# Optimization experiments

Hardware: AMD Instinct MI355X
Metric: run time of the kernel (lower is better)

## Reference

```python
import jax, jax.numpy as jnp
import numpy as np

B, N, D = 8, 1024, 768
H, Y, M = 12, 64, 3072  # heads, head_dim, hopfield memories (4*D)
STEPS = 12
ALPHA = 0.1
EPS = 1e-5


def setup_inputs() -> dict:
    key = jax.random.key(0)
    k0, k1, k2, k3 = jax.random.split(key, 4)
    return {
        "x": jax.random.normal(k0, (B, N, D), dtype=jnp.float32),
        "gamma": jnp.ones((D,), dtype=jnp.float32),
        "beta_ln": jnp.zeros((D,), dtype=jnp.float32),
        "Wq": jax.random.normal(k1, (H, Y, D), dtype=jnp.float32) / np.float32(np.sqrt(D)),
        "Wk": jax.random.normal(k2, (H, Y, D), dtype=jnp.float32) / np.float32(np.sqrt(D)),
        "xi": jax.random.normal(k3, (M, D), dtype=jnp.float32) / np.float32(np.sqrt(D)),
    }


def _layernorm(x, gamma, beta_ln):
    mu = jnp.mean(x, axis=-1, keepdims=True)
    var = jnp.var(x, axis=-1, keepdims=True)
    return gamma * (x - mu) * jax.lax.rsqrt(var + EPS) + beta_ln


def _energy(g, Wq, Wk, xi):
    # Energy attention: E^ATT = -(1/beta) * sum_{h,q} logsumexp_k(beta * <K_hk, Q_hq>)
    q = jnp.einsum('hyd,bnd->bhny', Wq, g)
    k = jnp.einsum('hyd,bnd->bhny', Wk, g)
    beta = jnp.asarray(1.0 / np.sqrt(Y), g.dtype)
    scores = beta * jnp.einsum('bhky,bhqy->bhkq', k, q)  # [B,H,N_k,N_q]
    e_att = -(1.0 / beta) * jnp.sum(jax.nn.logsumexp(scores, axis=2))
    # Hopfield energy: E^HN = -0.5 * sum relu(g @ xi^T)^2
    h = jnp.einsum('bnd,md->bnm', g, xi)
    e_hn = -0.5 * jnp.sum(jnp.square(jax.nn.relu(h)))
    return e_att + e_hn


def reference(x, gamma, beta_ln, Wq, Wk, xi):
    grad_e = jax.grad(_energy)
    def step(xc, _):
        g = _layernorm(xc, gamma, beta_ln)
        # gradient taken at g (not chained through LayerNorm), then SGD update
        xc = xc - ALPHA * grad_e(g, Wq, Wk, xi)
        return xc, None
    out, _ = jax.lax.scan(step, x, None, length=STEPS)
    return out
```

## Files before the change

### kernel.cpp

```cpp
#include <hip/hip_runtime.h>
#include <math.h>

#define H_ 12
#define STEPS_ 12
#define ALPHA_ 0.1f
#define EPS_ 1e-5f
#define BETA_ 0.125f
#define B2L_ 0.1803368801111204f
#define L2E_ 1.4426950408889634f
#define NTOK 8192

typedef unsigned short u16;
typedef __attribute__((ext_vector_type(8))) u16 u16x8;
typedef __attribute__((ext_vector_type(4))) u16 u16x4;
typedef __attribute__((ext_vector_type(4))) float f32x4;
typedef __attribute__((ext_vector_type(8))) __bf16 bf16x8;

#define MFMA __builtin_amdgcn_mfma_f32_16x16x32_bf16
#define EXP2F(x) __builtin_amdgcn_exp2f(x)

__device__ __forceinline__ u16 f2bf(float x) {
    unsigned u = __float_as_uint(x);
    u += 0x7FFFu + ((u >> 16) & 1u);
    return (u16)(u >> 16);
}
__device__ __forceinline__ float bf2f(u16 u) {
    return __uint_as_float(((unsigned)u) << 16);
}
__device__ __forceinline__ u16 f2bf_rz(float x) {
    return (u16)(__float_as_uint(x) >> 16);
}

__device__ __forceinline__ void gl2lds16(const u16* gsrc, u16* ldst) {
    __builtin_amdgcn_global_load_lds(
        (const __attribute__((address_space(1))) void*)gsrc,
        (__attribute__((address_space(3))) void*)ldst, 16, 0, 0);
}

#define RAW_BARRIER()   asm volatile("s_barrier" ::: "memory")
#define WAIT_VM(n)      asm volatile("s_waitcnt vmcnt(" #n ")" ::: "memory")
#define SCHED_FENCE()   __builtin_amdgcn_sched_barrier(0)

__global__ __launch_bounds__(256) void ln_kernel(const float* __restrict__ x,
    const float* __restrict__ gamma, const float* __restrict__ beta,
    u16* __restrict__ g)
{
    int row = blockIdx.x;
    const float* xr = x + (size_t)row * 768;
    u16* gr = g + (size_t)row * 768;
    int t = threadIdx.x;
    float v0 = xr[t], v1 = xr[t + 256], v2 = xr[t + 512];
    float s = v0 + v1 + v2;
    #pragma unroll
    for (int off = 32; off > 0; off >>= 1) s += __shfl_down(s, off);
    __shared__ float red[8];
    int wid = t >> 6, lane = t & 63;
    if (lane == 0) red[wid] = s;
    __syncthreads();
    if (t == 0) red[0] = (red[0] + red[1] + red[2] + red[3]) * (1.0f / 768.0f);
    __syncthreads();
    float mu = red[0];
    float d0 = v0 - mu, d1 = v1 - mu, d2 = v2 - mu;
    float ss = d0*d0 + d1*d1 + d2*d2;
    #pragma unroll
    for (int off = 32; off > 0; off >>= 1) ss += __shfl_down(ss, off);
    if (lane == 0) red[4 + wid] = ss;
    __syncthreads();
    if (t == 0) red[4] = rsqrtf((red[4] + red[5] + red[6] + red[7]) * (1.0f / 768.0f) + EPS_);
    __syncthreads();
    float rs = red[4];
    gr[t]       = f2bf(gamma[t]       * d0 * rs + beta[t]);
    gr[t + 256] = f2bf(gamma[t + 256] * d1 * rs + beta[t + 256]);
    gr[t + 512] = f2bf(gamma[t + 512] * d2 * rs + beta[t + 512]);
}

__global__ __launch_bounds__(192) void reduce_ln(const u16* __restrict__ part,
    float* __restrict__ xc, const float* __restrict__ gamma,
    const float* __restrict__ beta, u16* __restrict__ g)
{
    int row = blockIdx.x, t = threadIdx.x;
    const u16x4* p0 = (const u16x4*)(part + (size_t)row * 768);
    const u16x4* p1 = (const u16x4*)(part + (size_t)(8192 + row) * 768);
    f32x4* xr = (f32x4*)(xc + (size_t)row * 768);
    f32x4 v = xr[t];
    u16x4 a = p0[t], b = p1[t];
    #pragma unroll
    for (int e = 0; e < 4; ++e) v[e] = fmaf(ALPHA_, bf2f(a[e]) + bf2f(b[e]), v[e]);
    xr[t] = v;
    float s = (v[0] + v[1]) + (v[2] + v[3]);
    #pragma unroll
    for (int off = 32; off > 0; off >>= 1) s += __shfl_down(s, off);
    __shared__ float red[8];
    int wid = t >> 6, lane = t & 63;
    if (lane == 0) red[wid] = s;
    __syncthreads();
    if (t == 0) red[0] = (red[0] + red[1] + red[2]) * (1.0f / 768.0f);
    __syncthreads();
    float mu = red[0];
    f32x4 d;
    #pragma unroll
    for (int e = 0; e < 4; ++e) d[e] = v[e] - mu;
    float ss = (d[0]*d[0] + d[1]*d[1]) + (d[2]*d[2] + d[3]*d[3]);
    #pragma unroll
    for (int off = 32; off > 0; off >>= 1) ss += __shfl_down(ss, off);
    if (lane == 0) red[4 + wid] = ss;
    __syncthreads();
    if (t == 0) red[4] = rsqrtf((red[4] + red[5] + red[6]) * (1.0f / 768.0f) + EPS_);
    __syncthreads();
    float rs = red[4];
    const f32x4 gm = *(const f32x4*)&gamma[t * 4];
    const f32x4 bt = *(const f32x4*)&beta[t * 4];
    u16x4 o;
    #pragma unroll
    for (int e = 0; e < 4; ++e) o[e] = f2bf(fmaf(gm[e], d[e] * rs, bt[e]));
    *(u16x4*)&g[(size_t)row * 768 + t * 4] = o;
}

__global__ __launch_bounds__(256) void convert_bf(const float* __restrict__ src,
                                                  u16* __restrict__ dst, int n4)
{
    int i = blockIdx.x * 256 + threadIdx.x;
    if (i < n4) {
        f32x4 v = *(const f32x4*)&src[i * 4];
        u16x4 o;
        #pragma unroll
        for (int e = 0; e < 4; ++e) o[e] = f2bf(v[e]);
        *(u16x4*)&dst[i * 4] = o;
    }
}

__global__ __launch_bounds__(256) void transpose_bf(const float* __restrict__ Wq,
    const float* __restrict__ Wk, const float* __restrict__ xi, u16* __restrict__ out)
{
    __shared__ float tile[64][65];
    int rb = blockIdx.x * 64, cb = blockIdx.y * 64;
    const float* src;
    if (rb < 768) src = Wq + (size_t)rb * 768;
    else if (rb < 1536) src = Wk + (size_t)(rb - 768) * 768;
    else src = xi + (size_t)(rb - 1536) * 768;
    int t = threadIdx.x;
    #pragma unroll
    for (int it = 0; it < 4; ++it) {
        int r = (t >> 4) + 16 * it;
        f32x4 v = *(const f32x4*)&src[(size_t)r * 768 + cb + (t & 15) * 4];
        #pragma unroll
        for (int e = 0; e < 4; ++e) tile[r][(t & 15) * 4 + e] = v[e];
    }
    __syncthreads();
    #pragma unroll
    for (int it = 0; it < 4; ++it) {
        int cl = (t >> 4) + 16 * it;
        u16x4 o;
        #pragma unroll
        for (int e = 0; e < 4; ++e) o[e] = f2bf(tile[(t & 15) * 4 + e][cl]);
        *(u16x4*)&out[(size_t)(cb + cl) * 4608 + rb + (t & 15) * 4] = o;
    }
}


__global__ __launch_bounds__(512) void gemm_fwd(
    const u16* __restrict__ A,
    const u16* __restrict__ Bt,
    u16* __restrict__ qkb, u16* __restrict__ qkT, u16* __restrict__ midb)
{
    __shared__ __align__(16) u16 S[2][28672];
    const int t = threadIdx.x, w = t >> 6, l = t & 63, g = l >> 4, cid = l & 15;
    const int lr = l & 15, lc = l >> 4;
    const int wm = w >> 2, wn = w & 3;
    const int flat = blockIdx.x;
    const int xcd = flat & 7, slot = flat >> 3;
    const int nid = slot >> 2, mloc = slot & 3;
    const int bm = (xcd * 4 + mloc) * 256;
    const int bn = nid * 192;
    const int NT = 12;

    const u16* aS[4]; int ldA[4];
    #pragma unroll
    for (int j = 0; j < 4; ++j) {
        int rf = 2 * w + (j >> 1), kh = j & 1;
        aS[j] = A + (size_t)(bm + 16 * rf + lr) * 768 + 32 * kh + 8 * lc;
        ldA[j] = rf * 1024 + kh * 512 + l * 8;
    }
    const u16* bS[3]; int ldB[3];
    #pragma unroll
    for (int j = 0; j < 3; ++j) {
        int c = 3 * w + j, rf = c >> 1, kh = c & 1;
        bS[j] = Bt + (size_t)(bn + 16 * rf + lr) * 768 + 32 * kh + 8 * lc;
        ldB[j] = 16384 + rf * 1024 + kh * 512 + l * 8;
    }

    f32x4 acc[8][3] = {};
    bf16x8 afr[4][2], b0[2][2], b1[2];

    #pragma unroll
    for (int j = 0; j < 3; ++j) gl2lds16(bS[j], &S[0][ldB[j]]);
    #pragma unroll
    for (int j = 0; j < 4; ++j) gl2lds16(aS[j], &S[0][ldA[j]]);
    #pragma unroll
    for (int j = 0; j < 3; ++j) gl2lds16(bS[j] + 64, &S[1][ldB[j]]);
    WAIT_VM(3); RAW_BARRIER();

    #pragma unroll 1
    for (int tt = 0; tt < NT; ++tt) {
        const int bf = tt & 1, ob = bf ^ 1;
        const u16* Sa = &S[bf][0];
        const u16* Sb = &S[bf][16384];
        #define LDS_A(ii, hh) (*(const bf16x8*)&Sa[((wm * 8 + (ii)) * 128 + (hh) * 64 + l) * 8])
        #define LDS_B(jj, hh) (*(const bf16x8*)&Sb[((3 * wn + (jj)) * 128 + (hh) * 64 + l) * 8])
        #define MM(ii, jj, BF0, BF1) { \
            acc[ii][jj] = MFMA(afr[(ii) & 3][0], BF0, acc[ii][jj], 0, 0, 0); \
            acc[ii][jj] = MFMA(afr[(ii) & 3][1], BF1, acc[ii][jj], 0, 0, 0); }
        #pragma unroll
        for (int i = 0; i < 4; ++i) { afr[i][0] = LDS_A(i, 0); afr[i][1] = LDS_A(i, 1); }
        #pragma unroll
        for (int j = 0; j < 2; ++j) { b0[j][0] = LDS_B(j, 0); b0[j][1] = LDS_B(j, 1); }
        b1[0] = LDS_B(2, 0); b1[1] = LDS_B(2, 1);
        if (tt + 1 < NT) { gl2lds16(aS[0] + 64 * (tt + 1), &S[ob][ldA[0]]);
                           gl2lds16(aS[1] + 64 * (tt + 1), &S[ob][ldA[1]]);
                           gl2lds16(aS[2] + 64 * (tt + 1), &S[ob][ldA[2]]);
                           gl2lds16(aS[3] + 64 * (tt + 1), &S[ob][ldA[3]]); }
        RAW_BARRIER();
        __builtin_amdgcn_s_setprio(1);
        #pragma unroll
        for (int i = 0; i < 4; ++i) {
            MM(i, 0, b0[0][0], b0[0][1]);
            MM(i, 1, b0[1][0], b0[1][1]);
            MM(i, 2, b1[0],    b1[1]);
        }
        __builtin_amdgcn_s_setprio(0);
        SCHED_FENCE(); RAW_BARRIER();
        #pragma unroll
        for (int i = 0; i < 4; ++i) { afr[i][0] = LDS_A(4 + i, 0); afr[i][1] = LDS_A(4 + i, 1); }
        if (tt + 2 < NT) { gl2lds16(bS[0] + 64 * (tt + 2), &S[bf][ldB[0]]);
                           gl2lds16(bS[1] + 64 * (tt + 2), &S[bf][ldB[1]]);
                           gl2lds16(bS[2] + 64 * (tt + 2), &S[bf][ldB[2]]); }
        RAW_BARRIER();
        __builtin_amdgcn_s_setprio(1);
        #pragma unroll
        for (int i = 0; i < 4; ++i) {
            MM(4 + i, 0, b0[0][0], b0[0][1]);
            MM(4 + i, 1, b0[1][0], b0[1][1]);
            MM(4 + i, 2, b1[0],    b1[1]);
        }
        __builtin_amdgcn_s_setprio(0);
        SCHED_FENCE();
        if (tt < NT - 2)       { WAIT_VM(3); }
        else if (tt == NT - 2) { WAIT_VM(0); }
        RAW_BARRIER();
        #undef LDS_A
        #undef LDS_B
        #undef MM
    }

    if (bn < 1536) {
        int bidx = bm >> 10;
        #pragma unroll
        for (int i = 0; i < 8; ++i) {
            int tok = bm + wm * 128 + 16 * i + 4 * g;
            #pragma unroll
            for (int j = 0; j < 3; ++j) {
                int col = bn + wn * 48 + 16 * j + cid;
                int sel = col >= 768 ? 1 : 0;
                int cc = col - 768 * sel;
                int hh = cc >> 6, yy = cc & 63;
                u16x4 tv;
                #pragma unroll
                for (int r = 0; r < 4; ++r) {
                    u16 bv = f2bf(acc[i][j][r]);
                    tv[r] = bv;
                    qkb[(size_t)(tok + r) * 1536 + col] = bv;
                }
                *(u16x4*)&qkT[((((size_t)bidx * 12 + hh) * 2 + sel) * 64 + yy) * 1024 + (tok & 1023)] = tv;
            }
        }
    } else {
        #pragma unroll
        for (int i = 0; i < 8; ++i)
            #pragma unroll
            for (int r = 0; r < 4; ++r) {
                size_t row = bm + wm * 128 + 16 * i + 4 * g + r;
                #pragma unroll
                for (int j = 0; j < 3; ++j) {
                    int col = bn + wn * 48 + 16 * j + cid;
                    midb[row * 4608 + col] = f2bf(fmaxf(acc[i][j][r], 0.0f));
                }
            }
    }
}

__global__ __launch_bounds__(512) void gemm_upd(
    const u16* __restrict__ A,
    const u16* __restrict__ Bt,
    u16* __restrict__ part)
{
    __shared__ __align__(16) u16 S[2][28672];
    const int t = threadIdx.x, w = t >> 6, l = t & 63, g = l >> 4, cid = l & 15;
    const int lr = l & 15, lc = l >> 4;
    const int wm = w >> 2, wn = w & 3;
    const int flat = blockIdx.x;
    const int xcd = flat & 7, slot = flat >> 3;
    const int z = slot >> 4, rem = slot & 15;
    const int nid = rem >> 2, mloc = rem & 3;
    const int bm = (xcd * 4 + mloc) * 256, bn = nid * 192;
    const int kbeg = z * 2304;
    const int NT = 36;
    u16* out = part + (size_t)z * 8192 * 768;

    const u16* aS[4]; int ldA[4];
    #pragma unroll
    for (int j = 0; j < 4; ++j) {
        int rf = 2 * w + (j >> 1), kh = j & 1;
        aS[j] = A + (size_t)(bm + 16 * rf + lr) * 4608 + kbeg + 32 * kh + 8 * lc;
        ldA[j] = rf * 1024 + kh * 512 + l * 8;
    }
    const u16* bS[3]; int ldB[3];
    #pragma unroll
    for (int j = 0; j < 3; ++j) {
        int c = 3 * w + j, rf = c >> 1, kh = c & 1;
        bS[j] = Bt + (size_t)(bn + 16 * rf + lr) * 4608 + kbeg + 32 * kh + 8 * lc;
        ldB[j] = 16384 + rf * 1024 + kh * 512 + l * 8;
    }

    f32x4 acc[8][3] = {};
    bf16x8 afr[4][2], b0[2][2], b1[2];

    #pragma unroll
    for (int j = 0; j < 3; ++j) gl2lds16(bS[j], &S[0][ldB[j]]);
    #pragma unroll
    for (int j = 0; j < 4; ++j) gl2lds16(aS[j], &S[0][ldA[j]]);
    #pragma unroll
    for (int j = 0; j < 3; ++j) gl2lds16(bS[j] + 64, &S[1][ldB[j]]);
    WAIT_VM(3); RAW_BARRIER();

    #pragma unroll 1
    for (int tt = 0; tt < NT; ++tt) {
        const int bf = tt & 1, ob = bf ^ 1;
        const u16* Sa = &S[bf][0];
        const u16* Sb = &S[bf][16384];
        #define LDS_A(ii, hh) (*(const bf16x8*)&Sa[((wm * 8 + (ii)) * 128 + (hh) * 64 + l) * 8])
        #define LDS_B(jj, hh) (*(const bf16x8*)&Sb[((3 * wn + (jj)) * 128 + (hh) * 64 + l) * 8])
        #define MM(ii, jj, BF0, BF1) { \
            acc[ii][jj] = MFMA(afr[(ii) & 3][0], BF0, acc[ii][jj], 0, 0, 0); \
            acc[ii][jj] = MFMA(afr[(ii) & 3][1], BF1, acc[ii][jj], 0, 0, 0); }
        #pragma unroll
        for (int i = 0; i < 4; ++i) { afr[i][0] = LDS_A(i, 0); afr[i][1] = LDS_A(i, 1); }
        #pragma unroll
        for (int j = 0; j < 2; ++j) { b0[j][0] = LDS_B(j, 0); b0[j][1] = LDS_B(j, 1); }
        b1[0] = LDS_B(2, 0); b1[1] = LDS_B(2, 1);
        if (tt + 1 < NT) { gl2lds16(aS[0] + 64 * (tt + 1), &S[ob][ldA[0]]);
                           gl2lds16(aS[1] + 64 * (tt + 1), &S[ob][ldA[1]]);
                           gl2lds16(aS[2] + 64 * (tt + 1), &S[ob][ldA[2]]);
                           gl2lds16(aS[3] + 64 * (tt + 1), &S[ob][ldA[3]]); }
        RAW_BARRIER();
        __builtin_amdgcn_s_setprio(1);
        #pragma unroll
        for (int i = 0; i < 4; ++i) {
            MM(i, 0, b0[0][0], b0[0][1]);
            MM(i, 1, b0[1][0], b0[1][1]);
            MM(i, 2, b1[0],    b1[1]);
        }
        __builtin_amdgcn_s_setprio(0);
        SCHED_FENCE(); RAW_BARRIER();
        #pragma unroll
        for (int i = 0; i < 4; ++i) { afr[i][0] = LDS_A(4 + i, 0); afr[i][1] = LDS_A(4 + i, 1); }
        if (tt + 2 < NT) { gl2lds16(bS[0] + 64 * (tt + 2), &S[bf][ldB[0]]);
                           gl2lds16(bS[1] + 64 * (tt + 2), &S[bf][ldB[1]]);
                           gl2lds16(bS[2] + 64 * (tt + 2), &S[bf][ldB[2]]); }
        RAW_BARRIER();
        __builtin_amdgcn_s_setprio(1);
        #pragma unroll
        for (int i = 0; i < 4; ++i) {
            MM(4 + i, 0, b0[0][0], b0[0][1]);
            MM(4 + i, 1, b0[1][0], b0[1][1]);
            MM(4 + i, 2, b1[0],    b1[1]);
        }
        __builtin_amdgcn_s_setprio(0);
        SCHED_FENCE();
        if (tt < NT - 2)       { WAIT_VM(3); }
        else if (tt == NT - 2) { WAIT_VM(0); }
        RAW_BARRIER();
        #undef LDS_A
        #undef LDS_B
        #undef MM
    }

    #pragma unroll
    for (int i = 0; i < 8; ++i)
        #pragma unroll
        for (int r = 0; r < 4; ++r) {
            size_t row = bm + wm * 128 + 16 * i + 4 * g + r;
            #pragma unroll
            for (int j = 0; j < 3; ++j)
                out[row * 768 + bn + wn * 48 + 16 * j + cid] = f2bf(acc[i][j][r]);
        }
}

__global__ __launch_bounds__(256) void dq_kernel(const u16* __restrict__ qk,
    const u16* __restrict__ qkT, float* __restrict__ L, u16* __restrict__ mid)
{
    const int flat = blockIdx.x;
    const int xcd = flat & 7, slot = flat >> 3;
    const int bh = xcd * 12 + slot / 8;
    const int q0 = (slot % 8) << 7;
    const int b = bh / H_, h = bh % H_;
    const u16* qbase = qk + (size_t)b * 1024 * 1536 + h * 64;
    const u16* kbase = qbase + 768;
    const u16* ktg = qkT + ((size_t)bh * 2 + 1) * 64 * 1024;
    __shared__ __align__(16) u16 KB[2][8192];
    __shared__ __align__(16) u16 Ps[8192];
    const int t = threadIdx.x, w = t >> 6, l = t & 63, g = l >> 4, cid = l & 15;
    const int lr = l & 15, lc = l >> 4;

    #pragma unroll
    for (int h2 = 0; h2 < 2; ++h2)
        #pragma unroll
        for (int ch = 0; ch < 2; ++ch)
            gl2lds16(&qbase[(size_t)(q0 + 32 * w + 16 * h2 + lr) * 1536 + 32 * ch + 8 * lc],
                     &KB[0][(128 * (2 * w + h2) + 64 * ch + l) * 8]);
    __syncthreads();
    bf16x8 QF[2][2];
    #pragma unroll
    for (int jj = 0; jj < 2; ++jj)
        #pragma unroll
        for (int hh = 0; hh < 2; ++hh)
            QF[jj][hh] = *(const bf16x8*)&KB[0][(128 * (2 * w + jj) + 64 * hh + l) * 8];
    __syncthreads();

    auto stageK = [&](int buf, int kt) {
        #pragma unroll
        for (int ch = 0; ch < 2; ++ch) {
            gl2lds16(&kbase[(size_t)(kt * 64 + 16 * w + lr) * 1536 + 32 * ch + 8 * lc],
                     &KB[buf][(128 * w + 64 * ch + l) * 8]);
            gl2lds16(&ktg[(size_t)(16 * w + lr) * 1024 + kt * 64 + 32 * ch + 8 * lc],
                     &KB[buf][4096 + (128 * w + 64 * ch + l) * 8]);
        }
    };

    f32x4 acc[2][4] = {};
    float lrun[2] = {0.0f, 0.0f};

    stageK(0, 0); stageK(1, 1);
    #pragma unroll 1
    for (int kt = 0; kt < 16; ++kt) {
        if (kt == 15) { WAIT_VM(0); } else { WAIT_VM(4); }
        RAW_BARRIER();
        const int buf = kt & 1;
        const u16* Kn = &KB[buf][0];
        const u16* Kt = &KB[buf][4096];
        f32x4 s[4][2];
        #pragma unroll
        for (int i = 0; i < 4; ++i) {
            bf16x8 a0 = *(const bf16x8*)&Kn[(128 * i + l) * 8];
            bf16x8 a1 = *(const bf16x8*)&Kn[(128 * i + 64 + l) * 8];
            #pragma unroll
            for (int jj = 0; jj < 2; ++jj) {
                f32x4 z = {0.f, 0.f, 0.f, 0.f};
                z = MFMA(a0, QF[jj][0], z, 0, 0, 0);
                z = MFMA(a1, QF[jj][1], z, 0, 0, 0);
                s[i][jj] = z;
            }
        }
        #pragma unroll
        for (int jj = 0; jj < 2; ++jj) {
            float psum = 0.0f;
            #pragma unroll
            for (int i = 0; i < 4; ++i) {
                u16x4 pv;
                #pragma unroll
                for (int r = 0; r < 4; ++r) {
                    float p = EXP2F(s[i][jj][r] * B2L_);
                    psum += p;
                    pv[r] = f2bf_rz(p);
                }
                *(u16x4*)&Ps[(128 * (2 * w + jj) + 32 * i + 16 * (g >> 1) + cid) * 8 + 4 * (g & 1)] = pv;
            }
            psum += __shfl_xor(psum, 16);
            psum += __shfl_xor(psum, 32);
            lrun[jj] += psum;
        }
        #pragma unroll
        for (int jj = 0; jj < 2; ++jj) {
            bf16x8 p0 = *(const bf16x8*)&Ps[(128 * (2 * w + jj) + l) * 8];
            bf16x8 p1 = *(const bf16x8*)&Ps[(128 * (2 * w + jj) + 64 + l) * 8];
            #pragma unroll
            for (int j = 0; j < 4; ++j) {
                acc[jj][j] = MFMA(p0, *(const bf16x8*)&Kt[(128 * j + l) * 8], acc[jj][j], 0, 0, 0);
                acc[jj][j] = MFMA(p1, *(const bf16x8*)&Kt[(128 * j + 64 + l) * 8], acc[jj][j], 0, 0, 0);
            }
        }
        RAW_BARRIER();
        if (kt + 2 < 16) stageK(buf, kt + 2);
    }
    #pragma unroll
    for (int jj = 0; jj < 2; ++jj) {
        if (g == 0)
            L[(size_t)bh * 1024 + q0 + 32 * w + 16 * jj + cid] = __logf(lrun[jj]);
        float linv = 1.0f / lrun[jj];
        #pragma unroll
        for (int r = 0; r < 4; ++r) {
            float fr = __shfl(linv, 4 * g + r);
            int row = q0 + 32 * w + 16 * jj + 4 * g + r;
            #pragma unroll
            for (int j = 0; j < 4; ++j)
                mid[(size_t)(b * 1024 + row) * 4608 + h * 64 + 16 * j + cid] = f2bf(acc[jj][j][r] * fr);
        }
    }
}

__global__ __launch_bounds__(256) void dk_kernel(const u16* __restrict__ qk,
    const u16* __restrict__ qkT, const float* __restrict__ L, u16* __restrict__ mid)
{
    const int flat = blockIdx.x;
    const int xcd = flat & 7, slot = flat >> 3;
    const int bh = xcd * 12 + slot / 8;
    const int k0 = (slot % 8) << 7;
    const int b = bh / H_, h = bh % H_;
    const u16* qbase = qk + (size_t)b * 1024 * 1536 + h * 64;
    const u16* kbase = qbase + 768;
    const u16* qtg = qkT + ((size_t)bh * 2 + 0) * 64 * 1024;
    __shared__ __align__(16) u16 KB[2][8192];
    __shared__ __align__(16) u16 Ps[8192];
    const int t = threadIdx.x, w = t >> 6, l = t & 63, g = l >> 4, cid = l & 15;
    const int lr = l & 15, lc = l >> 4;

    #pragma unroll
    for (int h2 = 0; h2 < 2; ++h2)
        #pragma unroll
        for (int ch = 0; ch < 2; ++ch)
            gl2lds16(&kbase[(size_t)(k0 + 32 * w + 16 * h2 + lr) * 1536 + 32 * ch + 8 * lc],
                     &KB[0][(128 * (2 * w + h2) + 64 * ch + l) * 8]);
    __syncthreads();
    bf16x8 KF[2][2];
    #pragma unroll
    for (int jj = 0; jj < 2; ++jj)
        #pragma unroll
        for (int hh = 0; hh < 2; ++hh)
            KF[jj][hh] = *(const bf16x8*)&KB[0][(128 * (2 * w + jj) + 64 * hh + l) * 8];
    __syncthreads();

    auto stageQ = [&](int buf, int qt) {
        #pragma unroll
        for (int ch = 0; ch < 2; ++ch) {
            gl2lds16(&qbase[(size_t)(qt * 64 + 16 * w + lr) * 1536 + 32 * ch + 8 * lc],
                     &KB[buf][(128 * w + 64 * ch + l) * 8]);
            gl2lds16(&qtg[(size_t)(16 * w + lr) * 1024 + qt * 64 + 32 * ch + 8 * lc],
                     &KB[buf][4096 + (128 * w + 64 * ch + l) * 8]);
        }
    };

    f32x4 acc[2][4] = {};
    stageQ(0, 0); stageQ(1, 1);
    #pragma unroll 1
    for (int qt = 0; qt < 16; ++qt) {
        if (qt == 15) { WAIT_VM(0); } else { WAIT_VM(4); }
        RAW_BARRIER();
        const int buf = qt & 1;
        const u16* Qn = &KB[buf][0];
        const u16* Qt = &KB[buf][4096];
        #pragma unroll
        for (int i = 0; i < 4; ++i) {
            bf16x8 a0 = *(const bf16x8*)&Qn[(128 * i + l) * 8];
            bf16x8 a1 = *(const bf16x8*)&Qn[(128 * i + 64 + l) * 8];
            f32x4 lv = *(const f32x4*)&L[(size_t)bh * 1024 + qt * 64 + 16 * i + 4 * g];
            f32x4 lv2;
            #pragma unroll
            for (int r = 0; r < 4; ++r) lv2[r] = lv[r] * L2E_;
            #pragma unroll
            for (int jj = 0; jj < 2; ++jj) {
                f32x4 z = {0.f, 0.f, 0.f, 0.f};
                z = MFMA(a0, KF[jj][0], z, 0, 0, 0);
                z = MFMA(a1, KF[jj][1], z, 0, 0, 0);
                u16x4 pv;
                #pragma unroll
                for (int r = 0; r < 4; ++r)
                    pv[r] = f2bf_rz(EXP2F(fmaf(z[r], B2L_, -lv2[r])));
                *(u16x4*)&Ps[(128 * (2 * w + jj) + 32 * i + 16 * (g >> 1) + cid) * 8 + 4 * (g & 1)] = pv;
            }
        }
        #pragma unroll
        for (int jj = 0; jj < 2; ++jj) {
            bf16x8 p0 = *(const bf16x8*)&Ps[(128 * (2 * w + jj) + l) * 8];
            bf16x8 p1 = *(const bf16x8*)&Ps[(128 * (2 * w + jj) + 64 + l) * 8];
            #pragma unroll
            for (int j = 0; j < 4; ++j) {
                acc[jj][j] = MFMA(p0, *(const bf16x8*)&Qt[(128 * j + l) * 8], acc[jj][j], 0, 0, 0);
                acc[jj][j] = MFMA(p1, *(const bf16x8*)&Qt[(128 * j + 64 + l) * 8], acc[jj][j], 0, 0, 0);
            }
        }
        RAW_BARRIER();
        if (qt + 2 < 16) stageQ(buf, qt + 2);
    }
    #pragma unroll
    for (int jj = 0; jj < 2; ++jj)
        #pragma unroll
        for (int r = 0; r < 4; ++r) {
            int row = k0 + 32 * w + 16 * jj + 4 * g + r;
            #pragma unroll
            for (int j = 0; j < 4; ++j)
                mid[(size_t)(b * 1024 + row) * 4608 + 768 + h * 64 + 16 * j + cid] = f2bf(acc[jj][j][r]);
        }
}

extern "C" void kernel_launch(void* const* d_in, const int* in_sizes, int n_in,
                              void* d_out, int out_size, void* d_ws, size_t ws_size,
                              hipStream_t stream)
{
    const float* x     = (const float*)d_in[0];
    const float* gamma = (const float*)d_in[1];
    const float* betap = (const float*)d_in[2];
    const float* Wq    = (const float*)d_in[3];
    const float* Wk    = (const float*)d_in[4];
    const float* xi    = (const float*)d_in[5];
    float* xc = (float*)d_out;

    char* p = (char*)d_ws;
    u16* wcat_bf  = (u16*)p; p += (size_t)4608 * 768 * 2;
    u16* wcatT_bf = (u16*)p; p += (size_t)768 * 4608 * 2;
    u16* g_bf     = (u16*)p; p += (size_t)NTOK * 768 * 2;
    u16* qk_bf    = (u16*)p; p += (size_t)NTOK * 1536 * 2;
    u16* qkT_bf   = (u16*)p; p += (size_t)96 * 2 * 64 * 1024 * 2;
    u16* mid_bf   = (u16*)p; p += (size_t)NTOK * 4608 * 2;
    float* L      = (float*)p; p += (size_t)96 * 1024 * 4;
    u16* part = qk_bf;
    (void)ws_size; (void)in_sizes; (void)n_in; (void)out_size;

    hipMemcpyAsync(xc, x, (size_t)NTOK * 768 * 4, hipMemcpyDeviceToDevice, stream);

    convert_bf<<<576, 256, 0, stream>>>(Wq, wcat_bf, 147456);
    convert_bf<<<576, 256, 0, stream>>>(Wk, wcat_bf + 768 * 768, 147456);
    convert_bf<<<2304, 256, 0, stream>>>(xi, wcat_bf + 2 * 768 * 768, 589824);
    transpose_bf<<<dim3(72, 12), 256, 0, stream>>>(Wq, Wk, xi, wcatT_bf);

    ln_kernel<<<NTOK, 256, 0, stream>>>(x, gamma, betap, g_bf);

    for (int step = 0; step < STEPS_; ++step) {
        gemm_fwd<<<768, 512, 0, stream>>>(
            g_bf, wcat_bf, qk_bf, qkT_bf, mid_bf);
        dq_kernel<<<768, 256, 0, stream>>>(qk_bf, qkT_bf, L, mid_bf);
        dk_kernel<<<768, 256, 0, stream>>>(qk_bf, qkT_bf, L, mid_bf);
        gemm_upd<<<256, 512, 0, stream>>>(mid_bf, wcatT_bf, part);
        reduce_ln<<<NTOK, 192, 0, stream>>>(part, xc, gamma, betap, g_bf);
    }
}
```

Before: 3.036 ms.

## Make forward GEMM blocks loop over three N tiles in one launch

The forward GEMM now launches 256 blocks instead of 768. Each block walks three consecutive 192-column N tiles (576 columns) through one continuous software pipeline of 36 K-steps. Prefetch carries across tile boundaries, and the epilogue writes out and resets the accumulators after every 12 K-steps. The aim is to cut block launch and pipeline fill/drain overhead and to keep the A tile hot in cache, at the cost of fewer blocks (about one per CU) and epilogue stores that stall the pipeline mid-loop.

```diff
diff --git a/kernel.cpp b/kernel.cpp
--- a/kernel.cpp
+++ b/kernel.cpp
@@ -169,10 +169,11 @@
     const int wm = w >> 2, wn = w & 3;
     const int flat = blockIdx.x;
     const int xcd = flat & 7, slot = flat >> 3;
-    const int nid = slot >> 2, mloc = slot & 3;
+    const int ngrp = slot >> 2, mloc = slot & 3;
     const int bm = (xcd * 4 + mloc) * 256;
-    const int bn = nid * 192;
-    const int NT = 12;
+    const int bn0 = ngrp * 576;
+    const int NT = 36;
+    const int bidx = bm >> 10;
 
     const u16* aS[4]; int ldA[4];
     #pragma unroll
@@ -185,19 +186,68 @@
     #pragma unroll
     for (int j = 0; j < 3; ++j) {
         int c = 3 * w + j, rf = c >> 1, kh = c & 1;
-        bS[j] = Bt + (size_t)(bn + 16 * rf + lr) * 768 + 32 * kh + 8 * lc;
+        bS[j] = Bt + (size_t)(bn0 + 16 * rf + lr) * 768 + 32 * kh + 8 * lc;
         ldB[j] = 16384 + rf * 1024 + kh * 512 + l * 8;
     }
+
+    auto stageA = [&](int buf, int tau) {
+        int kt = tau - (tau / 12) * 12;
+        #pragma unroll
+        for (int j = 0; j < 4; ++j) gl2lds16(aS[j] + 64 * kt, &S[buf][ldA[j]]);
+    };
+    auto stageB = [&](int buf, int tau) {
+        int ni = tau / 12, kt = tau - ni * 12;
+        size_t off = (size_t)ni * 147456 + 64 * kt;
+        #pragma unroll
+        for (int j = 0; j < 3; ++j) gl2lds16(bS[j] + off, &S[buf][ldB[j]]);
+    };
 
     f32x4 acc[8][3] = {};
     bf16x8 afr[4][2], b0[2][2], b1[2];
 
-    #pragma unroll
-    for (int j = 0; j < 3; ++j) gl2lds16(bS[j], &S[0][ldB[j]]);
-    #pragma unroll
-    for (int j = 0; j < 4; ++j) gl2lds16(aS[j], &S[0][ldA[j]]);
-    #pragma unroll
-    for (int j = 0; j < 3; ++j) gl2lds16(bS[j] + 64, &S[1][ldB[j]]);
+    auto epilogue = [&](int ni) {
+        int bn = bn0 + ni * 192;
+        if (bn < 1536) {
+            #pragma unroll
+            for (int i = 0; i < 8; ++i) {
+                int tok = bm + wm * 128 + 16 * i + 4 * g;
+                #pragma unroll
+                for (int j = 0; j < 3; ++j) {
+                    int col = bn + wn * 48 + 16 * j + cid;
+                    int sel = col >= 768 ? 1 : 0;
+                    int cc = col - 768 * sel;
+                    int hh = cc >> 6, yy = cc & 63;
+                    u16x4 tv;
+                    #pragma unroll
+                    for (int r = 0; r < 4; ++r) {
+                        u16 bv = f2bf(acc[i][j][r]);
+                        tv[r] = bv;
+                        qkb[(size_t)(tok + r) * 1536 + col] = bv;
+                    }
+                    *(u16x4*)&qkT[((((size_t)bidx * 12 + hh) * 2 + sel) * 64 + yy) * 1024 + (tok & 1023)] = tv;
+                }
+            }
+        } else {
+            #pragma unroll
+            for (int i = 0; i < 8; ++i)
+                #pragma unroll
+                for (int r = 0; r < 4; ++r) {
+                    size_t row = bm + wm * 128 + 16 * i + 4 * g + r;
+                    #pragma unroll
+                    for (int j = 0; j < 3; ++j) {
+                        int col = bn + wn * 48 + 16 * j + cid;
+                        midb[row * 4608 + col] = f2bf(fmaxf(acc[i][j][r], 0.0f));
+                    }
+                }
+        }
+        #pragma unroll
+        for (int i = 0; i < 8; ++i)
+            #pragma unroll
+            for (int j = 0; j < 3; ++j)
+                acc[i][j] = (f32x4){0.f, 0.f, 0.f, 0.f};
+    };
+
+    stageB(0, 0); stageA(0, 0); stageB(1, 1);
     WAIT_VM(3); RAW_BARRIER();
 
     #pragma unroll 1
@@ -215,10 +265,7 @@
         #pragma unroll
         for (int j = 0; j < 2; ++j) { b0[j][0] = LDS_B(j, 0); b0[j][1] = LDS_B(j, 1); }
         b1[0] = LDS_B(2, 0); b1[1] = LDS_B(2, 1);
-        if (tt + 1 < NT) { gl2lds16(aS[0] + 64 * (tt + 1), &S[ob][ldA[0]]);
-                           gl2lds16(aS[1] + 64 * (tt + 1), &S[ob][ldA[1]]);
-                           gl2lds16(aS[2] + 64 * (tt + 1), &S[ob][ldA[2]]);
-                           gl2lds16(aS[3] + 64 * (tt + 1), &S[ob][ldA[3]]); }
+        if (tt + 1 < NT) stageA(ob, tt + 1);
         RAW_BARRIER();
         __builtin_amdgcn_s_setprio(1);
         #pragma unroll
@@ -231,9 +278,7 @@
         SCHED_FENCE(); RAW_BARRIER();
         #pragma unroll
         for (int i = 0; i < 4; ++i) { afr[i][0] = LDS_A(4 + i, 0); afr[i][1] = LDS_A(4 + i, 1); }
-        if (tt + 2 < NT) { gl2lds16(bS[0] + 64 * (tt + 2), &S[bf][ldB[0]]);
-                           gl2lds16(bS[1] + 64 * (tt + 2), &S[bf][ldB[1]]);
-                           gl2lds16(bS[2] + 64 * (tt + 2), &S[bf][ldB[2]]); }
+        if (tt + 2 < NT) stageB(bf, tt + 2);
         RAW_BARRIER();
         __builtin_amdgcn_s_setprio(1);
         #pragma unroll
@@ -250,41 +295,10 @@
         #undef LDS_A
         #undef LDS_B
         #undef MM
-    }
-
-    if (bn < 1536) {
-        int bidx = bm >> 10;
-        #pragma unroll
-        for (int i = 0; i < 8; ++i) {
-            int tok = bm + wm * 128 + 16 * i + 4 * g;
-            #pragma unroll
-            for (int j = 0; j < 3; ++j) {
-                int col = bn + wn * 48 + 16 * j + cid;
-                int sel = col >= 768 ? 1 : 0;
-                int cc = col - 768 * sel;
-                int hh = cc >> 6, yy = cc & 63;
-                u16x4 tv;
-                #pragma unroll
-                for (int r = 0; r < 4; ++r) {
-                    u16 bv = f2bf(acc[i][j][r]);
-                    tv[r] = bv;
-                    qkb[(size_t)(tok + r) * 1536 + col] = bv;
-                }
-                *(u16x4*)&qkT[((((size_t)bidx * 12 + hh) * 2 + sel) * 64 + yy) * 1024 + (tok & 1023)] = tv;
-            }
-        }
-    } else {
-        #pragma unroll
-        for (int i = 0; i < 8; ++i)
-            #pragma unroll
-            for (int r = 0; r < 4; ++r) {
-                size_t row = bm + wm * 128 + 16 * i + 4 * g + r;
-                #pragma unroll
-                for (int j = 0; j < 3; ++j) {
-                    int col = bn + wn * 48 + 16 * j + cid;
-                    midb[row * 4608 + col] = f2bf(fmaxf(acc[i][j][r], 0.0f));
-                }
-            }
+        {
+            int ni = tt / 12;
+            if (tt - ni * 12 == 11) epilogue(ni);
+        }
     }
 }
 
@@ -634,7 +648,7 @@
     ln_kernel<<<NTOK, 256, 0, stream>>>(x, gamma, betap, g_bf);
 
     for (int step = 0; step < STEPS_; ++step) {
-        gemm_fwd<<<768, 512, 0, stream>>>(
+        gemm_fwd<<<256, 512, 0, stream>>>(
             g_bf, wcat_bf, qk_bf, qkT_bf, mid_bf);
         dq_kernel<<<768, 256, 0, stream>>>(qk_bf, qkT_bf, L, mid_bf);
         dk_kernel<<<768, 256, 0, stream>>>(qk_bf, qkT_bf, L, mid_bf);
```

Result: slower. 3.738 ms (+23.2%).
